# Kernel optimization log

Hardware: AMD Instinct MI355X
Metric: run time of the kernel (lower is better)

The kernel has to match this reference:

```python
import jax, jax.numpy as jnp
import numpy as np

L, B, I, H = 1024, 128, 256, 512

def setup_inputs() -> dict:
    key = jax.random.key(0)
    k1, k2, k3, k4, k5 = jax.random.split(key, 5)
    s_i = 1.0 / np.sqrt(I)
    s_h = 1.0 / np.sqrt(H)
    return {
        "x": jax.random.normal(k1, (L, B, I), dtype=jnp.float32),
        "h": jax.random.normal(k2, (B, H), dtype=jnp.float32),
        "Wx": jax.random.uniform(k3, (H, I), jnp.float32, -s_i, s_i),
        "Wh": jax.random.uniform(k4, (H, H), jnp.float32, -s_h, s_h),
        "bh": jax.random.uniform(k5, (H,), jnp.float32, -s_h, s_h),
    }

def reference(x, h, Wx, Wh, bh):
    # Precompute input projection for all timesteps as one big GEMM:
    # (L,B,I) @ (I,H) -> (L,B,H)
    xproj = jnp.einsum("lbi,hi->lbh", x, Wx)

    def step(h_prev, xp_t):
        h_new = jnp.tanh(xp_t + h_prev @ Wh.T + bh)  # (B,H)
        return h_new, h_new

    _, h_seq = jax.lax.scan(step, h, xproj)
    return h_seq  # (L, B, H)
```

## Files before the change

### kernel.cpp

```cpp
#include <hip/hip_runtime.h>

#define L_DIM 1024
#define B_DIM 128
#define I_DIM 256
#define H_DIM 512

typedef unsigned short u16x8 __attribute__((ext_vector_type(8)));
typedef __bf16 bf16x8 __attribute__((ext_vector_type(8)));
typedef float f32x4 __attribute__((ext_vector_type(4)));
typedef unsigned long long u64;

static __device__ __forceinline__ unsigned short f2bf(float f) {
  unsigned u = __builtin_bit_cast(unsigned, f);
  u += 0x7FFFu + ((u >> 16) & 1u);
  return (unsigned short)(u >> 16);
}
static __device__ __forceinline__ float bf2f(unsigned short b) {
  return __builtin_bit_cast(float, ((unsigned)b) << 16);
}
static __device__ __forceinline__ bf16x8 ld_frag_g(const unsigned short* p, size_t idx8) {
  return __builtin_bit_cast(bf16x8, reinterpret_cast<const u16x8*>(p)[idx8]);
}

__global__ void pack_weights(const float* __restrict__ Wx, const float* __restrict__ Wh,
                             unsigned short* __restrict__ WxHi, unsigned short* __restrict__ WxLo,
                             unsigned short* __restrict__ WhHi, unsigned short* __restrict__ WhLo) {
  int tid = blockIdx.x * blockDim.x + threadIdx.x;
  if (tid < 32 * 8 * 64) {
    int lane = tid & 63, kt = (tid >> 6) & 7, nt = tid >> 9;
    int n = nt * 16 + (lane & 15), k0 = kt * 32 + (lane >> 4) * 8;
    const float* src = Wx + (size_t)n * I_DIM + k0;
    #pragma unroll
    for (int j = 0; j < 8; ++j) {
      float v = src[j];
      unsigned short hb = f2bf(v);
      WxHi[(size_t)tid * 8 + j] = hb;
      WxLo[(size_t)tid * 8 + j] = f2bf(v - bf2f(hb));
    }
  }
  if (tid < 32 * 16 * 64) {
    int lane = tid & 63, kt = (tid >> 6) & 15, nt = tid >> 10;
    int n = nt * 16 + (lane & 15), k0 = kt * 32 + (lane >> 4) * 8;
    const float* src = Wh + (size_t)n * H_DIM + k0;
    #pragma unroll
    for (int j = 0; j < 8; ++j) {
      float v = src[j];
      unsigned short hb = f2bf(v);
      WhHi[(size_t)tid * 8 + j] = hb;
      WhLo[(size_t)tid * 8 + j] = f2bf(v - bf2f(hb));
    }
  }
}

__global__ __launch_bounds__(256) void xproj_kernel(const float* __restrict__ x,
    const unsigned short* __restrict__ WxHi, const unsigned short* __restrict__ WxLo,
    const float* __restrict__ bh, float* __restrict__ out) {
  __shared__ unsigned short ahi[128][40];
  __shared__ unsigned short alo[128][40];
  const int tid = threadIdx.x, lane = tid & 63, wid = tid >> 6;
  const int mbase = blockIdx.x * 128, cbase = blockIdx.y * 128;
  const int wrow = (wid >> 1) * 64, wcol = (wid & 1) * 64;
  f32x4 acc[4][4] = {};
  const int srow = tid >> 1, shalf = (tid & 1) * 16;

  for (int kt = 0; kt < 8; ++kt) {
    const f32x4* src = reinterpret_cast<const f32x4*>(
        x + (size_t)(mbase + srow) * I_DIM + kt * 32 + shalf);
    f32x4 v[4];
    v[0] = src[0]; v[1] = src[1]; v[2] = src[2]; v[3] = src[3];
    u16x8 hh[2], ll[2];
    #pragma unroll
    for (int q = 0; q < 2; ++q) {
      #pragma unroll
      for (int e = 0; e < 8; ++e) {
        float f = v[q * 2 + (e >> 2)][e & 3];
        unsigned short hb = f2bf(f);
        hh[q][e] = hb;
        ll[q][e] = f2bf(f - bf2f(hb));
      }
    }
    __syncthreads();
    *reinterpret_cast<u16x8*>(&ahi[srow][shalf]) = hh[0];
    *reinterpret_cast<u16x8*>(&ahi[srow][shalf + 8]) = hh[1];
    *reinterpret_cast<u16x8*>(&alo[srow][shalf]) = ll[0];
    *reinterpret_cast<u16x8*>(&alo[srow][shalf + 8]) = ll[1];
    __syncthreads();

    bf16x8 amh[4], aml[4];
    #pragma unroll
    for (int m = 0; m < 4; ++m) {
      amh[m] = __builtin_bit_cast(bf16x8, *reinterpret_cast<const u16x8*>(
          &ahi[wrow + m * 16 + (lane & 15)][(lane >> 4) * 8]));
      aml[m] = __builtin_bit_cast(bf16x8, *reinterpret_cast<const u16x8*>(
          &alo[wrow + m * 16 + (lane & 15)][(lane >> 4) * 8]));
    }
    bf16x8 bhh[4], bll[4];
    #pragma unroll
    for (int n = 0; n < 4; ++n) {
      int ntg = (cbase + wcol) / 16 + n;
      size_t idx = (size_t)(ntg * 8 + kt) * 64 + lane;
      bhh[n] = ld_frag_g(WxHi, idx);
      bll[n] = ld_frag_g(WxLo, idx);
    }
    #pragma unroll
    for (int m = 0; m < 4; ++m) {
      #pragma unroll
      for (int n = 0; n < 4; ++n) {
        acc[m][n] = __builtin_amdgcn_mfma_f32_16x16x32_bf16(amh[m], bhh[n], acc[m][n], 0, 0, 0);
        acc[m][n] = __builtin_amdgcn_mfma_f32_16x16x32_bf16(aml[m], bhh[n], acc[m][n], 0, 0, 0);
        acc[m][n] = __builtin_amdgcn_mfma_f32_16x16x32_bf16(amh[m], bll[n], acc[m][n], 0, 0, 0);
      }
    }
  }

  #pragma unroll
  for (int n = 0; n < 4; ++n) {
    int col = cbase + wcol + n * 16 + (lane & 15);
    float bv = bh[col];
    #pragma unroll
    for (int m = 0; m < 4; ++m) {
      int rg = mbase + wrow + m * 16 + ((lane >> 4) << 2);
      #pragma unroll
      for (int r = 0; r < 4; ++r)
        out[(size_t)(rg + r) * H_DIM + col] = acc[m][n][r] + bv;
    }
  }
}

__global__ __launch_bounds__(256, 1) void rnn_kernel(const float* __restrict__ h0,
    const unsigned short* __restrict__ WhHi, const unsigned short* __restrict__ WhLo,
    unsigned int* __restrict__ tags, u64* __restrict__ gbuf,
    float* __restrict__ out) {
  __shared__ unsigned short hb[16 * 520 + 8];
  const int tid = threadIdx.x, lane = tid & 63, w = tid >> 6;
  const int g = blockIdx.x & 7, c = blockIdx.x >> 3;

  bf16x8 wfh[16], wfl[16];
  #pragma unroll
  for (int kt = 0; kt < 16; ++kt) {
    size_t idx = (size_t)((c * 4 + w) * 16 + kt) * 64 + lane;
    wfh[kt] = ld_frag_g(WhHi, idx);
    wfl[kt] = ld_frag_g(WhLo, idx);
  }
  for (int i = tid; i < 1024; i += 256) {
    int row = i >> 6, col0 = (i & 63) * 8;
    const f32x4* s = reinterpret_cast<const f32x4*>(h0 + (size_t)(g * 16 + row) * H_DIM + col0);
    f32x4 v0 = s[0], v1 = s[1];
    u16x8 hv;
    #pragma unroll
    for (int e = 0; e < 4; ++e) { hv[e] = f2bf(v0[e]); hv[4 + e] = f2bf(v1[e]); }
    *reinterpret_cast<u16x8*>(&hb[row * 520 + col0]) = hv;
  }
  __syncthreads();

  const int arow = lane & 15;
  const int aoff = (lane >> 4) * 8;
  const int drow = (lane >> 4) * 4;
  const int gcol = c * 64 + w * 16 + (lane & 15);
  const int rrow = tid >> 4, rcq = tid & 15;

  f32x4 xpv;
  {
    const size_t ob = ((size_t)0 * B_DIM + g * 16) * H_DIM;
    #pragma unroll
    for (int r = 0; r < 4; ++r)
      xpv[r] = out[ob + (size_t)(drow + r) * H_DIM + gcol];
  }

  for (int t = 0; t < L_DIM; ++t) {
    const size_t obase = ((size_t)t * B_DIM + g * 16) * H_DIM;

    bf16x8 af[16];
    #pragma unroll
    for (int kt = 0; kt < 16; ++kt)
      af[kt] = __builtin_bit_cast(bf16x8, *reinterpret_cast<const u16x8*>(
          &hb[arow * 520 + kt * 32 + aoff]));
    f32x4 a0 = {}, a1 = {}, a2 = {}, a3 = {};
    #pragma unroll
    for (int kt = 0; kt < 16; kt += 2) {
      a0 = __builtin_amdgcn_mfma_f32_16x16x32_bf16(af[kt], wfh[kt], a0, 0, 0, 0);
      a1 = __builtin_amdgcn_mfma_f32_16x16x32_bf16(af[kt], wfl[kt], a1, 0, 0, 0);
      a2 = __builtin_amdgcn_mfma_f32_16x16x32_bf16(af[kt + 1], wfh[kt + 1], a2, 0, 0, 0);
      a3 = __builtin_amdgcn_mfma_f32_16x16x32_bf16(af[kt + 1], wfl[kt + 1], a3, 0, 0, 0);
    }

    f32x4 xpn;
    {
      const int tn = (t < L_DIM - 1) ? t + 1 : t;
      const size_t ob = ((size_t)tn * B_DIM + g * 16) * H_DIM;
      #pragma unroll
      for (int r = 0; r < 4; ++r)
        xpn[r] = out[ob + (size_t)(drow + r) * H_DIM + gcol];
    }

    float hv[4];
    #pragma unroll
    for (int r = 0; r < 4; ++r) {
      float z = a0[r] + a1[r] + a2[r] + a3[r] + xpv[r];
      float e = __expf(2.0f * z);
      hv[r] = 1.0f - 2.0f / (e + 1.0f);
      out[obase + (size_t)(drow + r) * H_DIM + gcol] = hv[r];
    }
    xpv = xpn;
    if (t == L_DIM - 1) break;

    const unsigned buf = (t + 1) & 1;

    __syncthreads();
    #pragma unroll
    for (int r = 0; r < 4; ++r)
      hb[(drow + r) * 520 + gcol] = f2bf(hv[r]);
    __syncthreads();

    {
      u64 v = *reinterpret_cast<const u64*>(&hb[rrow * 520 + c * 64 + rcq * 4]);
      u64* dst = gbuf + ((size_t)(buf * 8 + g) * 8 + c) * 256 + tid;
      __hip_atomic_store(dst, v, __ATOMIC_RELAXED, __HIP_MEMORY_SCOPE_AGENT);
    }
    __syncthreads();
    if (tid == 0)
      __hip_atomic_store(tags + (buf * 8 + g) * 8 + c, (unsigned)(t + 1),
                         __ATOMIC_RELAXED, __HIP_MEMORY_SCOPE_AGENT);

    if (lane < 2) {
      unsigned s = 2 * w + lane;
      unsigned int* tp = tags + (buf * 8 + g) * 8 + s;
      while (__hip_atomic_load(tp, __ATOMIC_RELAXED, __HIP_MEMORY_SCOPE_AGENT) < (unsigned)(t + 1))
        __builtin_amdgcn_s_sleep(1);
    }
    asm volatile("" ::: "memory");

    #pragma unroll
    for (int si = 0; si < 2; ++si) {
      int s = 2 * w + si;
      if (s == c) continue;
      const u64* src = gbuf + ((size_t)(buf * 8 + g) * 8 + s) * 256;
      #pragma unroll
      for (int i = 0; i < 4; ++i) {
        int idx = i * 64 + lane;
        u64 v = __hip_atomic_load(src + idx, __ATOMIC_RELAXED, __HIP_MEMORY_SCOPE_AGENT);
        int row = idx >> 4, cq = idx & 15;
        *reinterpret_cast<u64*>(&hb[row * 520 + s * 64 + cq * 4]) = v;
      }
    }
    __syncthreads();
  }
}

extern "C" void kernel_launch(void* const* d_in, const int* in_sizes, int n_in,
                              void* d_out, int out_size, void* d_ws, size_t ws_size,
                              hipStream_t stream) {
  (void)in_sizes; (void)n_in; (void)out_size; (void)ws_size;
  const float* x  = (const float*)d_in[0];
  const float* h0 = (const float*)d_in[1];
  const float* Wx = (const float*)d_in[2];
  const float* Wh = (const float*)d_in[3];
  const float* bh = (const float*)d_in[4];
  float* out = (float*)d_out;

  unsigned short* WxHi = (unsigned short*)d_ws;
  unsigned short* WxLo = WxHi + 131072;
  unsigned short* WhHi = WxLo + 131072;
  unsigned short* WhLo = WhHi + 262144;
  unsigned int*   tags = (unsigned int*)((char*)d_ws + 1572864);
  u64*            gbuf = (u64*)((char*)d_ws + 1573888);

  hipMemsetAsync(tags, 0, 1024, stream);

  hipLaunchKernelGGL(pack_weights, dim3(128), dim3(256), 0, stream,
                     Wx, Wh, WxHi, WxLo, WhHi, WhLo);
  hipLaunchKernelGGL(xproj_kernel, dim3(1024, 4), dim3(256), 0, stream,
                     x, WxHi, WxLo, bh, out);
  hipLaunchKernelGGL(rnn_kernel, dim3(64), dim3(256), 0, stream,
                     h0, WhHi, WhLo, tags, gbuf, out);
}
```

Baseline: 3.308 ms.

## Publish hidden state per-wave directly from registers with per-wave flags

Each wave now packs its four bf16 outputs into a u64 and stores it straight to the global exchange buffer, then raises its own per-wave tag. The round trip through shared memory and the extra block barriers before publishing are gone. Consumers spin on seven tags in parallel lanes, pull all seven peer slices into registers, and scatter them into LDS with a transposed layout. Output stores and next-step xproj loads are moved between the publish and the wait so they overlap the inter-block latency. Correctness now rests on explicit waitcnt and sched_barrier ordering under relaxed atomics, and the tag array is twice as large.

```diff
diff --git a/kernel.cpp b/kernel.cpp
--- a/kernel.cpp
+++ b/kernel.cpp
@@ -131,7 +131,7 @@
     const unsigned short* __restrict__ WhHi, const unsigned short* __restrict__ WhLo,
     unsigned int* __restrict__ tags, u64* __restrict__ gbuf,
     float* __restrict__ out) {
-  __shared__ unsigned short hb[16 * 520 + 8];
+  __shared__ unsigned short hb[16 * 520];
   const int tid = threadIdx.x, lane = tid & 63, w = tid >> 6;
   const int g = blockIdx.x & 7, c = blockIdx.x >> 3;
 
@@ -157,15 +157,14 @@
   const int aoff = (lane >> 4) * 8;
   const int drow = (lane >> 4) * 4;
   const int gcol = c * 64 + w * 16 + (lane & 15);
-  const int rrow = tid >> 4, rcq = tid & 15;
+  const int pslot = (w * 16 + (lane & 15)) * 4 + (lane >> 4);
+  const int ccol = tid >> 2;
+  const int crow0 = (tid & 3) * 4;
 
   f32x4 xpv;
-  {
-    const size_t ob = ((size_t)0 * B_DIM + g * 16) * H_DIM;
-    #pragma unroll
-    for (int r = 0; r < 4; ++r)
-      xpv[r] = out[ob + (size_t)(drow + r) * H_DIM + gcol];
-  }
+  #pragma unroll
+  for (int r = 0; r < 4; ++r)
+    xpv[r] = out[(size_t)(g * 16 + drow + r) * H_DIM + gcol];
 
   for (int t = 0; t < L_DIM; ++t) {
     const size_t obase = ((size_t)t * B_DIM + g * 16) * H_DIM;
@@ -184,66 +183,72 @@
       a3 = __builtin_amdgcn_mfma_f32_16x16x32_bf16(af[kt + 1], wfl[kt + 1], a3, 0, 0, 0);
     }
 
-    f32x4 xpn;
-    {
-      const int tn = (t < L_DIM - 1) ? t + 1 : t;
-      const size_t ob = ((size_t)tn * B_DIM + g * 16) * H_DIM;
-      #pragma unroll
-      for (int r = 0; r < 4; ++r)
-        xpn[r] = out[ob + (size_t)(drow + r) * H_DIM + gcol];
-    }
-
-    float hv[4];
+    float hv[4]; unsigned short hu[4];
     #pragma unroll
     for (int r = 0; r < 4; ++r) {
       float z = a0[r] + a1[r] + a2[r] + a3[r] + xpv[r];
       float e = __expf(2.0f * z);
       hv[r] = 1.0f - 2.0f / (e + 1.0f);
-      out[obase + (size_t)(drow + r) * H_DIM + gcol] = hv[r];
-    }
-    xpv = xpn;
-    if (t == L_DIM - 1) break;
-
-    const unsigned buf = (t + 1) & 1;
-
-    __syncthreads();
-    #pragma unroll
-    for (int r = 0; r < 4; ++r)
-      hb[(drow + r) * 520 + gcol] = f2bf(hv[r]);
-    __syncthreads();
-
-    {
-      u64 v = *reinterpret_cast<const u64*>(&hb[rrow * 520 + c * 64 + rcq * 4]);
-      u64* dst = gbuf + ((size_t)(buf * 8 + g) * 8 + c) * 256 + tid;
-      __hip_atomic_store(dst, v, __ATOMIC_RELAXED, __HIP_MEMORY_SCOPE_AGENT);
-    }
-    __syncthreads();
-    if (tid == 0)
-      __hip_atomic_store(tags + (buf * 8 + g) * 8 + c, (unsigned)(t + 1),
+      hu[r] = f2bf(hv[r]);
+    }
+
+    if (t < L_DIM - 1) {
+      const unsigned buf = (t + 1) & 1;
+      u64 pv = (u64)hu[0] | ((u64)hu[1] << 16) | ((u64)hu[2] << 32) | ((u64)hu[3] << 48);
+      __hip_atomic_store(gbuf + (((size_t)(buf * 8 + g) * 8 + c) * 256 + pslot), pv,
                          __ATOMIC_RELAXED, __HIP_MEMORY_SCOPE_AGENT);
-
-    if (lane < 2) {
-      unsigned s = 2 * w + lane;
-      unsigned int* tp = tags + (buf * 8 + g) * 8 + s;
-      while (__hip_atomic_load(tp, __ATOMIC_RELAXED, __HIP_MEMORY_SCOPE_AGENT) < (unsigned)(t + 1))
-        __builtin_amdgcn_s_sleep(1);
-    }
-    asm volatile("" ::: "memory");
-
-    #pragma unroll
-    for (int si = 0; si < 2; ++si) {
-      int s = 2 * w + si;
-      if (s == c) continue;
-      const u64* src = gbuf + ((size_t)(buf * 8 + g) * 8 + s) * 256;
-      #pragma unroll
-      for (int i = 0; i < 4; ++i) {
-        int idx = i * 64 + lane;
-        u64 v = __hip_atomic_load(src + idx, __ATOMIC_RELAXED, __HIP_MEMORY_SCOPE_AGENT);
-        int row = idx >> 4, cq = idx & 15;
-        *reinterpret_cast<u64*>(&hb[row * 520 + s * 64 + cq * 4]) = v;
-      }
-    }
-    __syncthreads();
+      __builtin_amdgcn_sched_barrier(0);
+      asm volatile("s_waitcnt vmcnt(0)" ::: "memory");
+      __builtin_amdgcn_sched_barrier(0);
+      if (lane == 0)
+        __hip_atomic_store(tags + ((size_t)((buf * 8 + g) * 8 + c)) * 4 + w,
+                           (unsigned)(t + 1), __ATOMIC_RELAXED, __HIP_MEMORY_SCOPE_AGENT);
+
+      #pragma unroll
+      for (int r = 0; r < 4; ++r)
+        out[obase + (size_t)(drow + r) * H_DIM + gcol] = hv[r];
+      const size_t obn = ((size_t)(t + 1) * B_DIM + g * 16) * H_DIM;
+      #pragma unroll
+      for (int r = 0; r < 4; ++r)
+        xpv[r] = out[obn + (size_t)(drow + r) * H_DIM + gcol];
+
+      if (lane < 7) {
+        int s = lane + (lane >= c ? 1 : 0);
+        const unsigned int* tp = tags + ((size_t)((buf * 8 + g) * 8 + s)) * 4 + w;
+        while (__hip_atomic_load(tp, __ATOMIC_RELAXED, __HIP_MEMORY_SCOPE_AGENT)
+               < (unsigned)(t + 1)) {}
+      }
+      __builtin_amdgcn_sched_barrier(0);
+      u64 pul[7];
+      #pragma unroll
+      for (int si = 0; si < 7; ++si) {
+        int s = si + (si >= c ? 1 : 0);
+        pul[si] = __hip_atomic_load(gbuf + (((size_t)(buf * 8 + g) * 8 + s) * 256 + tid),
+                                    __ATOMIC_RELAXED, __HIP_MEMORY_SCOPE_AGENT);
+      }
+      __builtin_amdgcn_sched_barrier(0);
+      __builtin_amdgcn_s_barrier();
+      __builtin_amdgcn_sched_barrier(0);
+      #pragma unroll
+      for (int r = 0; r < 4; ++r)
+        hb[(drow + r) * 520 + gcol] = hu[r];
+      #pragma unroll
+      for (int si = 0; si < 7; ++si) {
+        int s = si + (si >= c ? 1 : 0);
+        #pragma unroll
+        for (int dr = 0; dr < 4; ++dr)
+          hb[(crow0 + dr) * 520 + s * 64 + ccol] = (unsigned short)(pul[si] >> (16 * dr));
+      }
+      __builtin_amdgcn_sched_barrier(0);
+      asm volatile("s_waitcnt lgkmcnt(0)" ::: "memory");
+      __builtin_amdgcn_sched_barrier(0);
+      __builtin_amdgcn_s_barrier();
+      __builtin_amdgcn_sched_barrier(0);
+    } else {
+      #pragma unroll
+      for (int r = 0; r < 4; ++r)
+        out[obase + (size_t)(drow + r) * H_DIM + gcol] = hv[r];
+    }
   }
 }
 
@@ -263,9 +268,9 @@
   unsigned short* WhHi = WxLo + 131072;
   unsigned short* WhLo = WhHi + 262144;
   unsigned int*   tags = (unsigned int*)((char*)d_ws + 1572864);
-  u64*            gbuf = (u64*)((char*)d_ws + 1573888);
-
-  hipMemsetAsync(tags, 0, 1024, stream);
+  u64*            gbuf = (u64*)((char*)d_ws + 1575936);
+
+  hipMemsetAsync(tags, 0, 2048, stream);
 
   hipLaunchKernelGGL(pack_weights, dim3(128), dim3(256), 0, stream,
                      Wx, Wh, WxHi, WxLo, WhHi, WhLo);
```

Result: faster. 3.002 ms (-9.3%).
